# Kernel tuning notes

Measured on AMD Instinct MI355X. Metric: run time of the kernel, lower is better.

The kernel has to match this reference:

```python
import jax, jax.numpy as jnp
import numpy as np

FUSION_WEIGHT = 0.5  # from version 'ca-fcat-0.5'

def setup_inputs() -> dict:
    key = jax.random.key(0)
    ks = jax.random.split(key, 6)
    B, N, D = 8, 2048, 1024
    scale = 1.0 / np.sqrt(D)
    return {
        "rgb":   jax.random.normal(ks[0], (B, N, D), dtype=jnp.float32),
        "freq":  jax.random.normal(ks[1], (B, N, D), dtype=jnp.float32),
        "ifreq": jax.random.normal(ks[2], (B, N, D), dtype=jnp.float32),
        "Wq": jax.random.normal(ks[3], (D, D), dtype=jnp.float32) * scale,
        "Wk": jax.random.normal(ks[4], (D, D), dtype=jnp.float32) * scale,
        "Wv": jax.random.normal(ks[5], (D, D), dtype=jnp.float32) * scale,
    }

def reference(rgb, freq, ifreq, Wq, Wk, Wv):
    # q/k/v projections (bias-free Linear). v path is dead code when use_freq=True
    # in the original module, so it is omitted (Wv/ifreq do not affect the output).
    q = jnp.einsum('bnd,de->bne', rgb, Wq)   # (B,N,E)
    k = jnp.einsum('bnd,de->bne', freq, Wk)  # (B,N,E)
    E = q.shape[-1]
    scores = jnp.einsum('bne,bme->bnm', q, k) / jnp.sqrt(jnp.float32(E))  # (B,N,N)
    attn = jax.nn.softmax(scores, axis=-1)
    # use_freq=True: reapply attention weights to the raw freq tensor
    attn_out = jnp.einsum('bnm,bmd->bnd', attn, freq)  # (B,N,D)
    # fusion 'cat' with weight 0.5 -> (B,N,2D)
    return jnp.concatenate([rgb, FUSION_WEIGHT * attn_out], axis=2)
```

## Files before the change

kernel.cpp:

```cpp
#include <hip/hip_runtime.h>
#include <hip/hip_bf16.h>
#include <stdint.h>


typedef __attribute__((ext_vector_type(8))) short   bf16x8;
typedef __attribute__((ext_vector_type(4))) float   f32x4;
typedef __attribute__((ext_vector_type(4))) int     i32x4;

static __device__ __forceinline__ unsigned short f2b(float f) {
  __hip_bfloat16 h = __float2bfloat16(f);
  return *reinterpret_cast<unsigned short*>(&h);
}
static __device__ __forceinline__ float b2f(unsigned short u) {
  unsigned int x = ((unsigned int)u) << 16;
  return __uint_as_float(x);
}
static __device__ __forceinline__ unsigned pq4(float a, float b, float c, float d, float s) {
  int qa = __float2int_rn(fminf(fmaxf(a * s, -127.f), 127.f)) & 255;
  int qb = __float2int_rn(fminf(fmaxf(b * s, -127.f), 127.f)) & 255;
  int qc = __float2int_rn(fminf(fmaxf(c * s, -127.f), 127.f)) & 255;
  int qd = __float2int_rn(fminf(fmaxf(d * s, -127.f), 127.f)) & 255;
  return (unsigned)qa | ((unsigned)qb << 8) | ((unsigned)qc << 16) | ((unsigned)qd << 24);
}

#define GLOAD_LDS16(g, l) \
  __builtin_amdgcn_global_load_lds( \
      (const __attribute__((address_space(1))) void*)(g), \
      (__attribute__((address_space(3))) void*)(l), 16, 0, 0)

__global__ __launch_bounds__(256) void cast_copy_rgb(
    const float* rgb, char* rB8, float* out) {
  size_t i = ((size_t)blockIdx.x * 256 + threadIdx.x) * 8;
  size_t m = i >> 10;
  int c = (int)(i & 1023);
  f32x4 a = *(const f32x4*)(rgb + i);
  f32x4 b = *(const f32x4*)(rgb + i + 4);
  *(f32x4*)(out + m * 2048 + c)     = a;
  *(f32x4*)(out + m * 2048 + c + 4) = b;
  uint2 w;
  w.x = pq4(a[0], a[1], a[2], a[3], 25.4f);
  w.y = pq4(b[0], b[1], b[2], b[3], 25.4f);
  *(uint2*)(rB8 + i) = w;
}

__global__ __launch_bounds__(256) void cast_w(
    const float* Wq, const float* Wk, __hip_bfloat16* wqB, __hip_bfloat16* wkB) {
  const float* src = blockIdx.y ? Wk : Wq;
  __hip_bfloat16* dst = blockIdx.y ? wkB : wqB;
  size_t i = ((size_t)blockIdx.x * 256 + threadIdx.x) * 8;
  f32x4 a = *(const f32x4*)(src + i);
  f32x4 b = *(const f32x4*)(src + i + 4);
  union { bf16x8 v; unsigned short u[8]; } cv;
#pragma unroll
  for (int j = 0; j < 4; ++j) { cv.u[j] = f2b(a[j]); cv.u[4 + j] = f2b(b[j]); }
  *(bf16x8*)(dst + i) = cv.v;
}

__global__ __launch_bounds__(256) void transpose_freq(
    const float* freq, char* fT8, char* doutB) {
  int b = blockIdx.z;
  const float* src = freq + (size_t)b * 2048 * 1024;
  int r0 = blockIdx.x * 32, c0 = blockIdx.y * 32;
  __shared__ float tile[32][33];
  int tid = threadIdx.x;
  int tx = tid & 31, ty = tid >> 5;
#pragma unroll
  for (int i = 0; i < 4; ++i)
    tile[ty + i * 8][tx] = src[(size_t)(r0 + ty + i * 8) * 1024 + c0 + tx];
  __syncthreads();
  {
    int a = tid >> 3, ch = (tid & 7) * 4;
    unsigned w = pq4(tile[a][ch], tile[a][ch + 1], tile[a][ch + 2], tile[a][ch + 3], 25.4f);
    *(unsigned*)(doutB + (size_t)(b * 2048 + r0 + a) * 8192 + 5120 + c0 + ch) = w;
  }
  {
    int bb = tid >> 3, w4 = (tid & 7) * 4;
    unsigned w = pq4(tile[w4][bb], tile[w4 + 1][bb], tile[w4 + 2][bb], tile[w4 + 3][bb], 25.4f);
    *(unsigned*)(fT8 + (size_t)b * 1024 * 2048 + (size_t)(c0 + bb) * 2048 + r0 + w4) = w;
  }
}

__global__ __launch_bounds__(256) void reduce_w(const float* slabs, char* Mt8) {
  size_t i = ((size_t)blockIdx.x * 256 + threadIdx.x) * 4;
  f32x4 a = *(const f32x4*)(slabs + i);
  f32x4 b = *(const f32x4*)(slabs + (size_t)(1 << 20) + i);
  f32x4 c = *(const f32x4*)(slabs + (size_t)(2 << 20) + i);
  f32x4 d = *(const f32x4*)(slabs + (size_t)(3 << 20) + i);
  unsigned w = pq4(a[0] + b[0] + c[0] + d[0], a[1] + b[1] + c[1] + d[1],
                   a[2] + b[2] + c[2] + d[2], a[3] + b[3] + c[3] + d[3], 812.8f);
  *(unsigned*)(Mt8 + i) = w;
}

template<bool C> struct AccSel      { using T = f32x4; };
template<>       struct AccSel<true>{ using T = i32x4; };

template<int MODE>
__global__ __launch_bounds__(512, 2) void gemm256(
    const void* pA0, const void* pB0, void* pC, const float* aux) {
  constexpr bool I8 = (MODE != 3);
  constexpr int NX = (MODE == 0) ? 64 : (MODE == 3) ? 4 : 8;
  constexpr int NY = (MODE == 1) ? 8 : 4;
  constexpr int NZ = (MODE == 0) ? 1 : (MODE == 3) ? 4 : 8;
  constexpr int NT = (MODE == 2) ? 16 : (MODE == 3) ? 4 : 8;
  constexpr long LDA = (MODE == 0) ? 1024 : (MODE == 1) ? 8192
                     : (MODE == 2) ? 4096 : 2048;
  constexpr long LDB = (MODE == 0) ? 1024 : (MODE == 1) ? 8192 : 2048;
  constexpr int NWG = NX * NY * NZ;
  using AccT = typename AccSel<I8>::T;

  int bid = blockIdx.x;
  int wg = (bid & 7) * (NWG >> 3) + (bid >> 3);
  int bx = wg % NX, by = (wg / NX) % NY, bz = wg / (NX * NY);
  const int row0 = bx * 256, col0 = by * 256;

  const int tid = threadIdx.x;
  const int wid = tid >> 6, l = tid & 63;
  const int wr = wid >> 2, wc = wid & 3;
  const int lm = l & 15, lk = (l >> 4) & 3;

  const char *A, *B;
  if constexpr (MODE == 0) {
    A = (const char*)pA0;
    B = (const char*)pB0;
  } else if constexpr (MODE == 1) {
    A = (const char*)pA0 + (size_t)bz*2048*8192 + 4096;
    B = (const char*)pA0 + (size_t)bz*2048*8192 + 5120;
  } else if constexpr (MODE == 2) {
    A = (const char*)pA0 + (size_t)bz*2048*4096;
    B = (const char*)pB0 + (size_t)bz*1024*2048;
  } else {
    A = (const char*)pA0 + (size_t)bz*512;
    B = (const char*)pB0 + (size_t)bz*512;
  }

  __shared__ __align__(16) unsigned char lds[131072];

  const int srow = l >> 2;
  const int scolB = ((l & 3) * 16) ^ ((l & 32) ? 32 : 0);
  const char* sA = A + (size_t)(row0 + wid*16 + srow) * LDA + scolB;
  const char* sB = B + (size_t)(col0 + wid*16 + srow) * LDB + scolB;

#define STAGE(mat, h, t) { \
    const char* _s = ((mat) ? sB : sA) \
        + (size_t)(h)*128*((mat) ? LDB : LDA) + (size_t)(t)*128; \
    unsigned _d = (unsigned)(((t)&1)*65536 + (mat)*32768 + (h)*16384 + wid*2048); \
    GLOAD_LDS16(_s,      lds + _d); \
    GLOAD_LDS16(_s + 64, lds + _d + 1024); }

  const int rdo = ((lm * 64) + (lk * 16)) ^ ((lm & 8) << 2);

  i32x4 aLo[4][2], aHi[4][2];
  i32x4 b01[2][2], b23[2][2];
  AccT acc[8][4];
#pragma unroll
  for (int m = 0; m < 8; ++m)
#pragma unroll
    for (int n = 0; n < 4; ++n) { AccT z = {}; acc[m][n] = z; }

#define LOAD_ALO(c) \
  _Pragma("unroll") for (int mi = 0; mi < 4; ++mi) \
  _Pragma("unroll") for (int s = 0; s < 2; ++s) \
    aLo[mi][s] = *(const i32x4*)(lds + (c)*65536 + wr*16384 \
                 + ((mi*2) + s)*1024 + rdo);
#define LOAD_AHI(c) \
  _Pragma("unroll") for (int mi = 0; mi < 4; ++mi) \
  _Pragma("unroll") for (int s = 0; s < 2; ++s) \
    aHi[mi][s] = *(const i32x4*)(lds + (c)*65536 + wr*16384 \
                 + (((4 + mi)*2) + s)*1024 + rdo);
#define LOAD_B01(c) \
  _Pragma("unroll") for (int ni = 0; ni < 2; ++ni) \
  _Pragma("unroll") for (int s = 0; s < 2; ++s) \
    b01[ni][s] = *(const i32x4*)(lds + (c)*65536 + 32768 + (wc>>1)*16384 \
                 + ((((wc&1)*4 + ni)*2) + s)*1024 + rdo);
#define LOAD_B23(c) \
  _Pragma("unroll") for (int ni = 0; ni < 2; ++ni) \
  _Pragma("unroll") for (int s = 0; s < 2; ++s) \
    b23[ni][s] = *(const i32x4*)(lds + (c)*65536 + 32768 + (wc>>1)*16384 \
                 + ((((wc&1)*4 + 2 + ni)*2) + s)*1024 + rdo);

#define MFMA_Q(af, bf, mo, no) \
  __builtin_amdgcn_s_setprio(1); \
  _Pragma("unroll") for (int mi = 0; mi < 4; ++mi) \
  _Pragma("unroll") for (int ni = 0; ni < 2; ++ni) \
  _Pragma("unroll") for (int s = 0; s < 2; ++s) { \
    if constexpr (I8) \
      acc[(mo) + mi][(no) + ni] = __builtin_amdgcn_mfma_i32_16x16x64_i8( \
          af[mi][s], bf[ni][s], acc[(mo) + mi][(no) + ni], 0, 0, 0); \
    else \
      acc[(mo) + mi][(no) + ni] = __builtin_amdgcn_mfma_f32_16x16x32_bf16( \
          __builtin_bit_cast(bf16x8, af[mi][s]), __builtin_bit_cast(bf16x8, bf[ni][s]), \
          acc[(mo) + mi][(no) + ni], 0, 0, 0); \
  } \
  __builtin_amdgcn_s_setprio(0);
#define BARR __builtin_amdgcn_s_barrier();
#define VMW2 asm volatile("s_waitcnt vmcnt(2)" ::: "memory");
#define VMW0 asm volatile("s_waitcnt vmcnt(0)" ::: "memory");

  STAGE(1, 0, 0) STAGE(0, 0, 0) STAGE(0, 1, 0) STAGE(1, 1, 0)
  STAGE(1, 0, 1)
  VMW2 BARR
  LOAD_ALO(0) LOAD_B01(0)
  STAGE(0, 0, 1)

  for (int g = 0; g < NT - 1; ++g) {
    const int cur = g & 1;
    const int nxt = cur ^ 1;
    const int tc2 = (g + 2 < NT) ? g + 2 : NT - 1;
    LOAD_B23(cur) STAGE(0, 1, g + 1)
    MFMA_Q(aLo, b01, 0, 0) BARR
    LOAD_AHI(cur) STAGE(1, 1, g + 1)
    MFMA_Q(aLo, b23, 0, 2) BARR
    STAGE(1, 0, tc2)
    MFMA_Q(aHi, b01, 4, 0) VMW2 BARR
    LOAD_ALO(nxt) LOAD_B01(nxt) STAGE(0, 0, tc2)
    MFMA_Q(aHi, b23, 4, 2) BARR
  }
  {
    const int cur = (NT - 1) & 1;
    LOAD_B23(cur)
    MFMA_Q(aLo, b01, 0, 0)
    LOAD_AHI(cur)
    MFMA_Q(aLo, b23, 0, 2)
    MFMA_Q(aHi, b01, 4, 0)
    MFMA_Q(aHi, b23, 4, 2)
  }
  VMW0

#pragma unroll
  for (int m = 0; m < 8; ++m)
#pragma unroll
    for (int n = 0; n < 4; ++n)
#pragma unroll
      for (int r = 0; r < 4; ++r) {
        float v;
        if constexpr (I8) v = (float)acc[m][n][r]; else v = acc[m][n][r];
        int grow = row0 + wr*128 + m*16 + lk*4 + r;
        int gcol = col0 + wc*64 + n*16 + lm;
        if constexpr (MODE == 0) {
          int q = __float2int_rn(fminf(fmaxf(v * 1.2303150e-3f, -127.f), 127.f));
          ((char*)pC)[(size_t)grow * 8192 + 4096 + gcol] = (char)q;
        } else if constexpr (MODE == 1) {
          __hip_bfloat16* Cb = (__hip_bfloat16*)pC + (size_t)bz*2048*2048;
          Cb[(size_t)grow * 2048 + gcol] = __float2bfloat16(v * 1.5500031e-3f);
        } else if constexpr (MODE == 2) {
          float* Cf = (float*)pC;
          Cf[((size_t)(bz*2048 + grow)) * 2048 + 1024 + gcol] =
              v * aux[bz*2048 + grow];
        } else {
          float* Cf = (float*)pC;
          Cf[(size_t)bz*1048576 + (size_t)grow*1024 + gcol] = v;
        }
      }
#undef STAGE
#undef LOAD_ALO
#undef LOAD_AHI
#undef LOAD_B01
#undef LOAD_B23
#undef MFMA_Q
#undef BARR
#undef VMW2
#undef VMW0
}

__global__ __launch_bounds__(256) void softmax_rows(char* Sbytes, float* rowfac) {
  const int row = blockIdx.x;
  const int t = threadIdx.x;
  char* rp = Sbytes + (size_t)row * 4096;
  uint4 raw = ((const uint4*)rp)[t];
  uint32_t w[4] = {raw.x, raw.y, raw.z, raw.w};
  float x[8];
#pragma unroll
  for (int i = 0; i < 4; ++i) {
    x[2*i]   = b2f((unsigned short)(w[i] & 0xffffu)) * 0.03125f;
    x[2*i+1] = b2f((unsigned short)(w[i] >> 16))     * 0.03125f;
  }
  float mx = x[0];
#pragma unroll
  for (int i = 1; i < 8; ++i) mx = fmaxf(mx, x[i]);
  for (int o = 32; o; o >>= 1) mx = fmaxf(mx, __shfl_xor(mx, o));
  __shared__ float redm[4], reds[4];
  int wid = t >> 6;
  if ((t & 63) == 0) redm[wid] = mx;
  __syncthreads();
  mx = fmaxf(fmaxf(redm[0], redm[1]), fmaxf(redm[2], redm[3]));
  float e[8], s = 0.f;
#pragma unroll
  for (int i = 0; i < 8; ++i) { e[i] = __expf(x[i] - mx); s += e[i]; }
  for (int o = 32; o; o >>= 1) s += __shfl_xor(s, o);
  if ((t & 63) == 0) reds[wid] = s;
  __syncthreads();
  s = reds[0] + reds[1] + reds[2] + reds[3];
  uint2 pw;
  pw.x = pw.y = 0;
#pragma unroll
  for (int j = 0; j < 4; ++j)
    pw.x |= (unsigned)(__float2int_rn(e[j] * 127.f) & 255) << (8 * j);
#pragma unroll
  for (int j = 0; j < 4; ++j)
    pw.y |= (unsigned)(__float2int_rn(e[4 + j] * 127.f) & 255) << (8 * j);
  ((uint2*)rp)[t] = pw;
  if (t == 0) rowfac[row] = 0.5f / (3225.8f * s);
}

extern "C" void kernel_launch(void* const* d_in, const int* in_sizes, int n_in,
                              void* d_out, int out_size, void* d_ws, size_t ws_size,
                              hipStream_t stream) {
  const float* rgb  = (const float*)d_in[0];
  const float* freq = (const float*)d_in[1];
  const float* Wq   = (const float*)d_in[3];
  const float* Wk   = (const float*)d_in[4];
  float* out = (float*)d_out;

  const size_t WS_NEED = (size_t)100 * 1024 * 1024;
  if (ws_size < WS_NEED) return;

  const size_t MB = 1 << 20;
  char* ws = (char*)d_ws;
  char*           S8     = ws;
  char*           rB8    = ws;
  float*          slabs  = (float*)(ws + 16 * MB);
  char*           Mt8    = ws + 32 * MB;
  __hip_bfloat16* wqB    = (__hip_bfloat16*)(ws + 34 * MB);
  __hip_bfloat16* wkB    = (__hip_bfloat16*)(ws + 36 * MB);
  char*           fT8    = ws + 64 * MB;
  float*          rowfac = (float*)(ws + 80 * MB);

  hipLaunchKernelGGL(cast_copy_rgb, dim3(8192), dim3(256), 0, stream, rgb, rB8, out);
  hipLaunchKernelGGL(cast_w, dim3(512, 2), dim3(256), 0, stream, Wq, Wk, wqB, wkB);
  hipLaunchKernelGGL(transpose_freq, dim3(64, 32, 8), dim3(256), 0, stream,
                     freq, fT8, (char*)out);
  hipLaunchKernelGGL((gemm256<3>), dim3(64), dim3(512), 0, stream,
                     (const void*)wkB, (const void*)wqB, (void*)slabs, (const float*)nullptr);
  hipLaunchKernelGGL(reduce_w, dim3(1024), dim3(256), 0, stream,
                     (const float*)slabs, Mt8);
  hipLaunchKernelGGL((gemm256<0>), dim3(256), dim3(512), 0, stream,
                     (const void*)rB8, (const void*)Mt8, (void*)out, (const float*)nullptr);
  hipLaunchKernelGGL((gemm256<1>), dim3(512), dim3(512), 0, stream,
                     (const void*)out, (const void*)nullptr, (void*)S8, (const float*)nullptr);
  hipLaunchKernelGGL(softmax_rows, dim3(16384), dim3(256), 0, stream, S8, rowfac);
  hipLaunchKernelGGL((gemm256<2>), dim3(256), dim3(512), 0, stream,
                     (const void*)S8, (const void*)fT8, (void*)out, (const float*)rowfac);
}
```

Baseline: 208.2 us.

## Merge prep kernels, int8 weight GEMM, fp16 scores, 256x512 score tiles

Folds the three preprocessing kernels (rgb copy/quantize, weight cast, freq transpose) into a single launch. The Wq/Wk product switches from a bf16 MFMA to an int8 MFMA with integer slabs. The score buffer changes from bf16 to fp16. Each MODE-1 workgroup now covers two 256-column tiles in one pipelined loop with a mid-loop epilogue, which halves that grid. The aim is fewer launches, a cheaper weight GEMM and better A-tile reuse, at the cost of int8 quantization error on the weights.

After: 227.0 us (median of 2 runs). 1.09x slower.

```diff
diff --git a/kernel.cpp b/kernel.cpp
--- a/kernel.cpp
+++ b/kernel.cpp
@@ -7,10 +7,6 @@
 typedef __attribute__((ext_vector_type(4))) float   f32x4;
 typedef __attribute__((ext_vector_type(4))) int     i32x4;
 
-static __device__ __forceinline__ unsigned short f2b(float f) {
-  __hip_bfloat16 h = __float2bfloat16(f);
-  return *reinterpret_cast<unsigned short*>(&h);
-}
 static __device__ __forceinline__ float b2f(unsigned short u) {
   unsigned int x = ((unsigned int)u) << 16;
   return __uint_as_float(x);
@@ -22,96 +18,110 @@
   int qd = __float2int_rn(fminf(fmaxf(d * s, -127.f), 127.f)) & 255;
   return (unsigned)qa | ((unsigned)qb << 8) | ((unsigned)qc << 16) | ((unsigned)qd << 24);
 }
+static __device__ __forceinline__ unsigned short f2h(float f) {
+  union { _Float16 h; unsigned short u; } cv;
+  cv.h = (_Float16)f;
+  return cv.u;
+}
+static __device__ __forceinline__ float h2f(unsigned short u) {
+  union { _Float16 h; unsigned short u; } cv;
+  cv.u = u;
+  return (float)cv.h;
+}
 
 #define GLOAD_LDS16(g, l) \
   __builtin_amdgcn_global_load_lds( \
       (const __attribute__((address_space(1))) void*)(g), \
       (__attribute__((address_space(3))) void*)(l), 16, 0, 0)
 
-__global__ __launch_bounds__(256) void cast_copy_rgb(
-    const float* rgb, char* rB8, float* out) {
-  size_t i = ((size_t)blockIdx.x * 256 + threadIdx.x) * 8;
-  size_t m = i >> 10;
-  int c = (int)(i & 1023);
-  f32x4 a = *(const f32x4*)(rgb + i);
-  f32x4 b = *(const f32x4*)(rgb + i + 4);
-  *(f32x4*)(out + m * 2048 + c)     = a;
-  *(f32x4*)(out + m * 2048 + c + 4) = b;
-  uint2 w;
-  w.x = pq4(a[0], a[1], a[2], a[3], 25.4f);
-  w.y = pq4(b[0], b[1], b[2], b[3], 25.4f);
-  *(uint2*)(rB8 + i) = w;
-}
-
-__global__ __launch_bounds__(256) void cast_w(
-    const float* Wq, const float* Wk, __hip_bfloat16* wqB, __hip_bfloat16* wkB) {
-  const float* src = blockIdx.y ? Wk : Wq;
-  __hip_bfloat16* dst = blockIdx.y ? wkB : wqB;
-  size_t i = ((size_t)blockIdx.x * 256 + threadIdx.x) * 8;
-  f32x4 a = *(const f32x4*)(src + i);
-  f32x4 b = *(const f32x4*)(src + i + 4);
-  union { bf16x8 v; unsigned short u[8]; } cv;
-#pragma unroll
-  for (int j = 0; j < 4; ++j) { cv.u[j] = f2b(a[j]); cv.u[4 + j] = f2b(b[j]); }
-  *(bf16x8*)(dst + i) = cv.v;
-}
-
-__global__ __launch_bounds__(256) void transpose_freq(
-    const float* freq, char* fT8, char* doutB) {
-  int b = blockIdx.z;
-  const float* src = freq + (size_t)b * 2048 * 1024;
-  int r0 = blockIdx.x * 32, c0 = blockIdx.y * 32;
+__global__ __launch_bounds__(256) void prep(
+    const float* rgb, const float* freq, const float* Wq, const float* Wk,
+    float* out, char* rB8, char* wq8, char* wk8, char* fT8, char* doutB) {
+  const int z = blockIdx.x;
+  const int tid = threadIdx.x;
   __shared__ float tile[32][33];
-  int tid = threadIdx.x;
-  int tx = tid & 31, ty = tid >> 5;
-#pragma unroll
-  for (int i = 0; i < 4; ++i)
-    tile[ty + i * 8][tx] = src[(size_t)(r0 + ty + i * 8) * 1024 + c0 + tx];
-  __syncthreads();
-  {
-    int a = tid >> 3, ch = (tid & 7) * 4;
-    unsigned w = pq4(tile[a][ch], tile[a][ch + 1], tile[a][ch + 2], tile[a][ch + 3], 25.4f);
-    *(unsigned*)(doutB + (size_t)(b * 2048 + r0 + a) * 8192 + 5120 + c0 + ch) = w;
-  }
-  {
-    int bb = tid >> 3, w4 = (tid & 7) * 4;
-    unsigned w = pq4(tile[w4][bb], tile[w4 + 1][bb], tile[w4 + 2][bb], tile[w4 + 3][bb], 25.4f);
-    *(unsigned*)(fT8 + (size_t)b * 1024 * 2048 + (size_t)(c0 + bb) * 2048 + r0 + w4) = w;
-  }
-}
-
-__global__ __launch_bounds__(256) void reduce_w(const float* slabs, char* Mt8) {
+
+  if (z < 8192) {
+    size_t i = ((size_t)z * 256 + tid) * 8;
+    size_t m = i >> 10;
+    int c = (int)(i & 1023);
+    f32x4 a = *(const f32x4*)(rgb + i);
+    f32x4 b = *(const f32x4*)(rgb + i + 4);
+    *(f32x4*)(out + m * 2048 + c)     = a;
+    *(f32x4*)(out + m * 2048 + c + 4) = b;
+    uint2 w;
+    w.x = pq4(a[0], a[1], a[2], a[3], 25.4f);
+    w.y = pq4(b[0], b[1], b[2], b[3], 25.4f);
+    *(uint2*)(rB8 + i) = w;
+  } else if (z < 9216) {
+    int zz = z - 8192;
+    const float* src = (zz >= 512) ? Wk : Wq;
+    char* dst = (zz >= 512) ? wk8 : wq8;
+    size_t i = ((size_t)(zz & 511) * 256 + tid) * 8;
+    f32x4 a = *(const f32x4*)(src + i);
+    f32x4 b = *(const f32x4*)(src + i + 4);
+    uint2 w;
+    w.x = pq4(a[0], a[1], a[2], a[3], 812.8f);
+    w.y = pq4(b[0], b[1], b[2], b[3], 812.8f);
+    *(uint2*)(dst + i) = w;
+  } else {
+    int zz = z - 9216;
+    int b = zz >> 11;
+    int rem = zz & 2047;
+    int r0 = (rem >> 5) * 32, c0 = (rem & 31) * 32;
+    const float* src = freq + (size_t)b * 2048 * 1024;
+    int tx = tid & 31, ty = tid >> 5;
+#pragma unroll
+    for (int i = 0; i < 4; ++i)
+      tile[ty + i * 8][tx] = src[(size_t)(r0 + ty + i * 8) * 1024 + c0 + tx];
+    __syncthreads();
+    {
+      int a = tid >> 3, ch = (tid & 7) * 4;
+      unsigned w = pq4(tile[a][ch], tile[a][ch + 1], tile[a][ch + 2], tile[a][ch + 3], 25.4f);
+      *(unsigned*)(doutB + (size_t)(b * 2048 + r0 + a) * 8192 + 5120 + c0 + ch) = w;
+    }
+    {
+      int bb = tid >> 3, w4 = (tid & 7) * 4;
+      unsigned w = pq4(tile[w4][bb], tile[w4 + 1][bb], tile[w4 + 2][bb], tile[w4 + 3][bb], 25.4f);
+      *(unsigned*)(fT8 + (size_t)b * 1024 * 2048 + (size_t)(c0 + bb) * 2048 + r0 + w4) = w;
+    }
+  }
+}
+
+__global__ __launch_bounds__(256) void reduce_w(const int* slabs, char* Mt8) {
   size_t i = ((size_t)blockIdx.x * 256 + threadIdx.x) * 4;
-  f32x4 a = *(const f32x4*)(slabs + i);
-  f32x4 b = *(const f32x4*)(slabs + (size_t)(1 << 20) + i);
-  f32x4 c = *(const f32x4*)(slabs + (size_t)(2 << 20) + i);
-  f32x4 d = *(const f32x4*)(slabs + (size_t)(3 << 20) + i);
-  unsigned w = pq4(a[0] + b[0] + c[0] + d[0], a[1] + b[1] + c[1] + d[1],
-                   a[2] + b[2] + c[2] + d[2], a[3] + b[3] + c[3] + d[3], 812.8f);
+  i32x4 a = *(const i32x4*)(slabs + i);
+  i32x4 b = *(const i32x4*)(slabs + (size_t)(1 << 20) + i);
+  i32x4 c = *(const i32x4*)(slabs + (size_t)(2 << 20) + i);
+  i32x4 d = *(const i32x4*)(slabs + (size_t)(3 << 20) + i);
+  const float inv = 1.0f / 812.8f;
+  unsigned w = pq4((float)(a[0] + b[0] + c[0] + d[0]), (float)(a[1] + b[1] + c[1] + d[1]),
+                   (float)(a[2] + b[2] + c[2] + d[2]), (float)(a[3] + b[3] + c[3] + d[3]), inv);
   *(unsigned*)(Mt8 + i) = w;
 }
-
-template<bool C> struct AccSel      { using T = f32x4; };
-template<>       struct AccSel<true>{ using T = i32x4; };
 
 template<int MODE>
 __global__ __launch_bounds__(512, 2) void gemm256(
     const void* pA0, const void* pB0, void* pC, const float* aux) {
-  constexpr bool I8 = (MODE != 3);
   constexpr int NX = (MODE == 0) ? 64 : (MODE == 3) ? 4 : 8;
-  constexpr int NY = (MODE == 1) ? 8 : 4;
+  constexpr int NY = (MODE == 2) ? 4 : (MODE == 3) ? 4 : (MODE == 1) ? 4 : 4;
   constexpr int NZ = (MODE == 0) ? 1 : (MODE == 3) ? 4 : 8;
-  constexpr int NT = (MODE == 2) ? 16 : (MODE == 3) ? 4 : 8;
+  constexpr int NT = (MODE == 2) ? 16 : (MODE == 3) ? 2 : 8;
+  constexpr int NV = (MODE == 1) ? 16 : NT;
+  constexpr int KM  = (MODE == 1) ? 7 : 255;
+  constexpr int KSH = (MODE == 1) ? 3 : 8;
   constexpr long LDA = (MODE == 0) ? 1024 : (MODE == 1) ? 8192
-                     : (MODE == 2) ? 4096 : 2048;
-  constexpr long LDB = (MODE == 0) ? 1024 : (MODE == 1) ? 8192 : 2048;
+                     : (MODE == 2) ? 4096 : 1024;
+  constexpr long LDB = (MODE == 0) ? 1024 : (MODE == 1) ? 8192
+                     : (MODE == 2) ? 2048 : 1024;
+  constexpr long REPB = (MODE == 1) ? 256 * LDB : 0;
   constexpr int NWG = NX * NY * NZ;
-  using AccT = typename AccSel<I8>::T;
 
   int bid = blockIdx.x;
   int wg = (bid & 7) * (NWG >> 3) + (bid >> 3);
   int bx = wg % NX, by = (wg / NX) % NY, bz = wg / (NX * NY);
-  const int row0 = bx * 256, col0 = by * 256;
+  const int row0 = bx * 256;
+  const int col0 = (MODE == 1) ? by * 512 : by * 256;
 
   const int tid = threadIdx.x;
   const int wid = tid >> 6, l = tid & 63;
@@ -129,8 +139,8 @@
     A = (const char*)pA0 + (size_t)bz*2048*4096;
     B = (const char*)pB0 + (size_t)bz*1024*2048;
   } else {
-    A = (const char*)pA0 + (size_t)bz*512;
-    B = (const char*)pB0 + (size_t)bz*512;
+    A = (const char*)pA0 + (size_t)bz*256;
+    B = (const char*)pB0 + (size_t)bz*256;
   }
 
   __shared__ __align__(16) unsigned char lds[131072];
@@ -140,10 +150,11 @@
   const char* sA = A + (size_t)(row0 + wid*16 + srow) * LDA + scolB;
   const char* sB = B + (size_t)(col0 + wid*16 + srow) * LDB + scolB;
 
-#define STAGE(mat, h, t) { \
+#define STAGE(mat, h, vt) { \
     const char* _s = ((mat) ? sB : sA) \
-        + (size_t)(h)*128*((mat) ? LDB : LDA) + (size_t)(t)*128; \
-    unsigned _d = (unsigned)(((t)&1)*65536 + (mat)*32768 + (h)*16384 + wid*2048); \
+        + (size_t)(h)*128*((mat) ? LDB : LDA) + (size_t)((vt) & KM)*128 \
+        + ((mat) ? (size_t)((vt) >> KSH) * REPB : 0); \
+    unsigned _d = (unsigned)(((vt)&1)*65536 + (mat)*32768 + (h)*16384 + wid*2048); \
     GLOAD_LDS16(_s,      lds + _d); \
     GLOAD_LDS16(_s + 64, lds + _d + 1024); }
 
@@ -151,11 +162,11 @@
 
   i32x4 aLo[4][2], aHi[4][2];
   i32x4 b01[2][2], b23[2][2];
-  AccT acc[8][4];
+  i32x4 acc[8][4];
 #pragma unroll
   for (int m = 0; m < 8; ++m)
 #pragma unroll
-    for (int n = 0; n < 4; ++n) { AccT z = {}; acc[m][n] = z; }
+    for (int n = 0; n < 4; ++n) { i32x4 z = {}; acc[m][n] = z; }
 
 #define LOAD_ALO(c) \
   _Pragma("unroll") for (int mi = 0; mi < 4; ++mi) \
@@ -182,19 +193,36 @@
   __builtin_amdgcn_s_setprio(1); \
   _Pragma("unroll") for (int mi = 0; mi < 4; ++mi) \
   _Pragma("unroll") for (int ni = 0; ni < 2; ++ni) \
-  _Pragma("unroll") for (int s = 0; s < 2; ++s) { \
-    if constexpr (I8) \
-      acc[(mo) + mi][(no) + ni] = __builtin_amdgcn_mfma_i32_16x16x64_i8( \
-          af[mi][s], bf[ni][s], acc[(mo) + mi][(no) + ni], 0, 0, 0); \
-    else \
-      acc[(mo) + mi][(no) + ni] = __builtin_amdgcn_mfma_f32_16x16x32_bf16( \
-          __builtin_bit_cast(bf16x8, af[mi][s]), __builtin_bit_cast(bf16x8, bf[ni][s]), \
-          acc[(mo) + mi][(no) + ni], 0, 0, 0); \
-  } \
+  _Pragma("unroll") for (int s = 0; s < 2; ++s) \
+    acc[(mo) + mi][(no) + ni] = __builtin_amdgcn_mfma_i32_16x16x64_i8( \
+        af[mi][s], bf[ni][s], acc[(mo) + mi][(no) + ni], 0, 0, 0); \
   __builtin_amdgcn_s_setprio(0);
 #define BARR __builtin_amdgcn_s_barrier();
 #define VMW2 asm volatile("s_waitcnt vmcnt(2)" ::: "memory");
 #define VMW0 asm volatile("s_waitcnt vmcnt(0)" ::: "memory");
+
+#define EPI(rep) { \
+    _Pragma("unroll") for (int m = 0; m < 8; ++m) \
+    _Pragma("unroll") for (int n = 0; n < 4; ++n) \
+    _Pragma("unroll") for (int r = 0; r < 4; ++r) { \
+      int grow = row0 + wr*128 + m*16 + lk*4 + r; \
+      int gcol = col0 + (rep)*256 + wc*64 + n*16 + lm; \
+      if constexpr (MODE == 0) { \
+        float v = (float)acc[m][n][r]; \
+        int q = __float2int_rn(fminf(fmaxf(v * 1.2303150e-3f, -127.f), 127.f)); \
+        ((char*)pC)[(size_t)grow * 8192 + 4096 + gcol] = (char)q; \
+      } else if constexpr (MODE == 1) { \
+        unsigned short* Ch = (unsigned short*)pC + (size_t)bz*2048*2048; \
+        Ch[(size_t)grow * 2048 + gcol] = f2h((float)acc[m][n][r] * 1.5500031e-3f); \
+      } else if constexpr (MODE == 2) { \
+        float* Cf = (float*)pC; \
+        Cf[((size_t)(bz*2048 + grow)) * 2048 + 1024 + gcol] = \
+            (float)acc[m][n][r] * aux[bz*2048 + grow]; \
+      } else { \
+        int* Ci = (int*)pC; \
+        Ci[(size_t)bz*1048576 + (size_t)grow*1024 + gcol] = acc[m][n][r]; \
+      } \
+    } }
 
   STAGE(1, 0, 0) STAGE(0, 0, 0) STAGE(0, 1, 0) STAGE(1, 1, 0)
   STAGE(1, 0, 1)
@@ -202,10 +230,19 @@
   LOAD_ALO(0) LOAD_B01(0)
   STAGE(0, 0, 1)
 
-  for (int g = 0; g < NT - 1; ++g) {
+  for (int g = 0; g < NV - 1; ++g) {
+    if constexpr (MODE == 1) {
+      if (g == 8) {
+        EPI(0)
+#pragma unroll
+        for (int m = 0; m < 8; ++m)
+#pragma unroll
+          for (int n = 0; n < 4; ++n) { i32x4 z = {}; acc[m][n] = z; }
+      }
+    }
     const int cur = g & 1;
     const int nxt = cur ^ 1;
-    const int tc2 = (g + 2 < NT) ? g + 2 : NT - 1;
+    const int tc2 = (g + 2 < NV) ? g + 2 : NV - 1;
     LOAD_B23(cur) STAGE(0, 1, g + 1)
     MFMA_Q(aLo, b01, 0, 0) BARR
     LOAD_AHI(cur) STAGE(1, 1, g + 1)
@@ -216,7 +253,7 @@
     MFMA_Q(aHi, b23, 4, 2) BARR
   }
   {
-    const int cur = (NT - 1) & 1;
+    const int cur = (NV - 1) & 1;
     LOAD_B23(cur)
     MFMA_Q(aLo, b01, 0, 0)
     LOAD_AHI(cur)
@@ -226,31 +263,8 @@
   }
   VMW0
 
-#pragma unroll
-  for (int m = 0; m < 8; ++m)
-#pragma unroll
-    for (int n = 0; n < 4; ++n)
-#pragma unroll
-      for (int r = 0; r < 4; ++r) {
-        float v;
-        if constexpr (I8) v = (float)acc[m][n][r]; else v = acc[m][n][r];
-        int grow = row0 + wr*128 + m*16 + lk*4 + r;
-        int gcol = col0 + wc*64 + n*16 + lm;
-        if constexpr (MODE == 0) {
-          int q = __float2int_rn(fminf(fmaxf(v * 1.2303150e-3f, -127.f), 127.f));
-          ((char*)pC)[(size_t)grow * 8192 + 4096 + gcol] = (char)q;
-        } else if constexpr (MODE == 1) {
-          __hip_bfloat16* Cb = (__hip_bfloat16*)pC + (size_t)bz*2048*2048;
-          Cb[(size_t)grow * 2048 + gcol] = __float2bfloat16(v * 1.5500031e-3f);
-        } else if constexpr (MODE == 2) {
-          float* Cf = (float*)pC;
-          Cf[((size_t)(bz*2048 + grow)) * 2048 + 1024 + gcol] =
-              v * aux[bz*2048 + grow];
-        } else {
-          float* Cf = (float*)pC;
-          Cf[(size_t)bz*1048576 + (size_t)grow*1024 + gcol] = v;
-        }
-      }
+  if constexpr (MODE == 1) { EPI(1) } else { EPI(0) }
+
 #undef STAGE
 #undef LOAD_ALO
 #undef LOAD_AHI
@@ -260,6 +274,7 @@
 #undef BARR
 #undef VMW2
 #undef VMW0
+#undef EPI
 }
 
 __global__ __launch_bounds__(256) void softmax_rows(char* Sbytes, float* rowfac) {
@@ -271,8 +286,8 @@
   float x[8];
 #pragma unroll
   for (int i = 0; i < 4; ++i) {
-    x[2*i]   = b2f((unsigned short)(w[i] & 0xffffu)) * 0.03125f;
-    x[2*i+1] = b2f((unsigned short)(w[i] >> 16))     * 0.03125f;
+    x[2*i]   = h2f((unsigned short)(w[i] & 0xffffu)) * 0.03125f;
+    x[2*i+1] = h2f((unsigned short)(w[i] >> 16))     * 0.03125f;
   }
   float mx = x[0];
 #pragma unroll
@@ -316,26 +331,24 @@
 
   const size_t MB = 1 << 20;
   char* ws = (char*)d_ws;
-  char*           S8     = ws;
-  char*           rB8    = ws;
-  float*          slabs  = (float*)(ws + 16 * MB);
-  char*           Mt8    = ws + 32 * MB;
-  __hip_bfloat16* wqB    = (__hip_bfloat16*)(ws + 34 * MB);
-  __hip_bfloat16* wkB    = (__hip_bfloat16*)(ws + 36 * MB);
-  char*           fT8    = ws + 64 * MB;
-  float*          rowfac = (float*)(ws + 80 * MB);
-
-  hipLaunchKernelGGL(cast_copy_rgb, dim3(8192), dim3(256), 0, stream, rgb, rB8, out);
-  hipLaunchKernelGGL(cast_w, dim3(512, 2), dim3(256), 0, stream, Wq, Wk, wqB, wkB);
-  hipLaunchKernelGGL(transpose_freq, dim3(64, 32, 8), dim3(256), 0, stream,
-                     freq, fT8, (char*)out);
+  char*  S8     = ws;
+  char*  rB8    = ws;
+  int*   slabs  = (int*)(ws + 16 * MB);
+  char*  Mt8    = ws + 32 * MB;
+  char*  wq8    = ws + 34 * MB;
+  char*  wk8    = ws + 35 * MB;
+  char*  fT8    = ws + 64 * MB;
+  float* rowfac = (float*)(ws + 80 * MB);
+
+  hipLaunchKernelGGL(prep, dim3(25600), dim3(256), 0, stream,
+                     rgb, freq, Wq, Wk, out, rB8, wq8, wk8, fT8, (char*)out);
   hipLaunchKernelGGL((gemm256<3>), dim3(64), dim3(512), 0, stream,
-                     (const void*)wkB, (const void*)wqB, (void*)slabs, (const float*)nullptr);
+                     (const void*)wk8, (const void*)wq8, (void*)slabs, (const float*)nullptr);
   hipLaunchKernelGGL(reduce_w, dim3(1024), dim3(256), 0, stream,
-                     (const float*)slabs, Mt8);
+                     (const int*)slabs, Mt8);
   hipLaunchKernelGGL((gemm256<0>), dim3(256), dim3(512), 0, stream,
                      (const void*)rB8, (const void*)Mt8, (void*)out, (const float*)nullptr);
-  hipLaunchKernelGGL((gemm256<1>), dim3(512), dim3(512), 0, stream,
+  hipLaunchKernelGGL((gemm256<1>), dim3(256), dim3(512), 0, stream,
                      (const void*)out, (const void*)nullptr, (void*)S8, (const float*)nullptr);
   hipLaunchKernelGGL(softmax_rows, dim3(16384), dim3(256), 0, stream, S8, rowfac);
   hipLaunchKernelGGL((gemm256<2>), dim3(256), dim3(512), 0, stream,
```
